# Kernel tuning notes

Hardware: AMD Instinct MI355X
Metric: run time of the kernel (lower is better)

The kernel has to match this reference:

```python
import jax, jax.numpy as jnp
import numpy as np

B, N_LR, N_HR, D, NH, L, K = 16, 256, 512, 512, 8, 4, 4
FF = 4 * D

def _ln(x, g, b):
    m = jnp.mean(x, -1, keepdims=True)
    v = jnp.var(x, -1, keepdims=True)
    return (x - m) * jax.lax.rsqrt(v + 1e-5) * g + b

def _gelu(x):
    return jax.nn.gelu(x, approximate=False)  # torch nn.GELU default = exact

def _attn(x, qkvW, qkvb, projW, projb, bias):
    b, n, d = x.shape
    hd = d // NH
    qkv = (x @ qkvW + qkvb).reshape(b, n, 3, NH, hd).transpose(2, 0, 3, 1, 4)
    q, k, v = qkv[0], qkv[1], qkv[2]
    a = jnp.einsum('bhnd,bhmd->bhnm', q, k) * (hd ** -0.5)
    if bias is not None:
        a = a + bias
    a = jax.nn.softmax(a, axis=-1)
    o = jnp.einsum('bhnm,bhmd->bhnd', a, v).transpose(0, 2, 1, 3).reshape(b, n, d)
    return o @ projW + projb

def _ffn(x, W1, b1, W2, b2):
    return _gelu(x @ W1 + b1) @ W2 + b2

def setup_inputs() -> dict:
    key = jax.random.key(0)
    ks = iter(jax.random.split(key, 64))
    def rn(shape, s=0.02):
        return jax.random.normal(next(ks), shape, jnp.float32) * s
    inp = {}
    A = rn((B, N_LR, N_LR), 1.0)
    A = 0.5 * (A + A.transpose(0, 2, 1))  # symmetric weighted adjacency
    inp['A_lr'] = A
    inp['X_lr'] = A  # node features = adjacency rows, as in the original model
    inp['ip_W'] = rn((N_LR, D)); inp['ip_b'] = jnp.zeros(D)
    inp['ip_g'] = jnp.ones(D); inp['ip_bt'] = jnp.zeros(D)
    inp['e_n1g'] = jnp.ones((L, D)); inp['e_n1b'] = jnp.zeros((L, D))
    inp['e_qkvW'] = rn((L, D, 3 * D)); inp['e_qkvb'] = jnp.zeros((L, 3 * D))
    inp['e_projW'] = rn((L, D, D)); inp['e_projb'] = jnp.zeros((L, D))
    inp['e_ebW'] = rn((L, NH), 1.0); inp['e_ebs'] = jnp.full((L,), 0.1)
    inp['e_n2g'] = jnp.ones((L, D)); inp['e_n2b'] = jnp.zeros((L, D))
    inp['e_f1W'] = rn((L, D, FF)); inp['e_f1b'] = jnp.zeros((L, FF))
    inp['e_f2W'] = rn((L, FF, D)); inp['e_f2b'] = jnp.zeros((L, D))
    inp['encn_g'] = jnp.ones(D); inp['encn_b'] = jnp.zeros(D)
    inp['up1W'] = rn((N_LR, N_HR)); inp['up1b'] = jnp.zeros(N_HR)
    inp['up2W'] = rn((N_HR, N_HR)); inp['up2b'] = jnp.zeros(N_HR)
    inp['r_n1g'] = jnp.ones(D); inp['r_n1b'] = jnp.zeros(D)
    inp['r_qkvW'] = rn((D, 3 * D)); inp['r_qkvb'] = jnp.zeros(3 * D)
    inp['r_projW'] = rn((D, D)); inp['r_projb'] = jnp.zeros(D)
    inp['r_n2g'] = jnp.ones(D); inp['r_n2b'] = jnp.zeros(D)
    inp['r_f1W'] = rn((D, FF)); inp['r_f1b'] = jnp.zeros(FF)
    inp['r_f2W'] = rn((FF, D)); inp['r_f2b'] = jnp.zeros(D)
    inp['hrn_g'] = jnp.ones(D); inp['hrn_b'] = jnp.zeros(D)
    inp['dec_W'] = rn((K, D, D)); inp['dec_b'] = jnp.full((1,), 3.0)
    return inp

def reference(A_lr, X_lr, ip_W, ip_b, ip_g, ip_bt, e_n1g, e_n1b, e_qkvW, e_qkvb, e_projW, e_projb, e_ebW, e_ebs, e_n2g, e_n2b, e_f1W, e_f1b, e_f2W, e_f2b, encn_g, encn_b, up1W, up1b, up2W, up2b, r_n1g, r_n1b, r_qkvW, r_qkvb, r_projW, r_projb, r_n2g, r_n2b, r_f1W, r_f1b, r_f2W, r_f2b, hrn_g, hrn_b, dec_W, dec_b):
    # input_proj: Linear -> LayerNorm -> GELU (dropout is identity in eval)
    H = _gelu(_ln(X_lr @ ip_W + ip_b, ip_g, ip_bt))  # (B, n_lr, D)
    # encoder: pre-norm blocks with additive per-head edge bias in softmax
    for l in range(L):
        bias = e_ebs[l] * A_lr[:, None, :, :] * e_ebW[l][None, :, None, None]  # (B,NH,N,N)
        H = H + _attn(_ln(H, e_n1g[l], e_n1b[l]), e_qkvW[l], e_qkvb[l], e_projW[l], e_projb[l], bias)
        H = H + _ffn(_ln(H, e_n2g[l], e_n2b[l]), e_f1W[l], e_f1b[l], e_f2W[l], e_f2b[l])
    H = _ln(H, encn_g, encn_b)
    # upsample n_lr -> n_hr along node axis (applied on transposed H)
    Ht = H.transpose(0, 2, 1)                      # (B, D, n_lr)
    Ht = _gelu(Ht @ up1W + up1b) @ up2W + up2b     # (B, D, n_hr)
    H = Ht.transpose(0, 2, 1)                      # (B, n_hr, D)
    # HR refinement: standard pre-norm self-attention block
    H = H + _attn(_ln(H, r_n1g, r_n1b), r_qkvW, r_qkvb, r_projW, r_projb, None)
    H = H + _ffn(_ln(H, r_n2g, r_n2b), r_f1W, r_f1b, r_f2W, r_f2b)
    H = _ln(H, hrn_g, hrn_b)
    # bilinear multi-head decoder: mean_k H W_k H^T, symmetrized
    A_pred = jnp.einsum('bnd,kde,bme->bnm', H, dec_W, H) / K
    A_pred = 0.5 * (A_pred + A_pred.transpose(0, 2, 1))
    iu, ju = np.triu_indices(N_HR, k=1)
    pred = A_pred[:, iu, ju]                        # (B, n_hr*(n_hr-1)/2)
    return jax.nn.softplus(pred + dec_b[0])
```

## Files before the change

### kernel.cpp

```cpp
#include <hip/hip_runtime.h>
#include <hip/hip_bf16.h>
#include <math.h>

#define DEV __device__ __forceinline__

typedef __attribute__((ext_vector_type(8))) short bf16x8;
typedef __attribute__((ext_vector_type(4))) short s16x4;
typedef __attribute__((ext_vector_type(4))) float f32x4;

DEV float gelu_f(float x) {
  float u = 1.5957691f * x * (1.0f + 0.044715f * x * x);
  return x / (1.0f + __expf(-u));
}

DEV short bf16s(float x) {
  __hip_bfloat16 v = __float2bfloat16(x);
  return *reinterpret_cast<short*>(&v);
}

DEV void async16(void* lds, const void* g) {
  __builtin_amdgcn_global_load_lds(
      (const __attribute__((address_space(1))) unsigned int*)g,
      (__attribute__((address_space(3))) unsigned int*)lds, 16, 0, 0);
}

__global__ __launch_bounds__(256) void conv2_kernel(
    const float* __restrict__ X1, __hip_bfloat16* __restrict__ Y1,
    const float* __restrict__ X2, __hip_bfloat16* __restrict__ Y2, int n) {
  int i = blockIdx.x * 256 + threadIdx.x;
  if (i < n) {
    Y1[i] = __float2bfloat16(X1[i]);
    Y2[i] = __float2bfloat16(X2[i]);
  }
}

struct CvArgs {
  const float* s[11];
  __hip_bfloat16* d[11];
};

__global__ __launch_bounds__(256) void multi_tconv_kernel(CvArgs a) {
  const int Rj[11] = {256, 512, 512, 512, 2048, 256, 512, 512, 512, 512, 2048};
  const int Cj[11] = {512, 1536, 512, 2048, 512, 512, 512, 1536, 512, 2048, 512};
  const int Nj[11] = {1, 4, 4, 4, 4, 1, 1, 1, 1, 1, 1};
  __shared__ float t[32][33];
  int rem = blockIdx.x, j = 0;
  for (; j < 11; ++j) {
    int tj = (Rj[j] >> 5) * (Cj[j] >> 5) * Nj[j];
    if (rem < tj) break;
    rem -= tj;
  }
  const int R = Rj[j], C = Cj[j];
  const int perb = (R >> 5) * (C >> 5);
  const int z = rem / perb;
  const int tt = rem % perb;
  const int tc = C >> 5;
  const int r0 = (tt / tc) << 5, c0 = (tt % tc) << 5;
  const float* xb = a.s[j] + (size_t)z * R * C;
  __hip_bfloat16* yb = a.d[j] + (size_t)z * R * C;
  int tx = threadIdx.x & 31, ty = threadIdx.x >> 5;
  for (int i = ty; i < 32; i += 8) t[i][tx] = xb[(size_t)(r0 + i) * C + c0 + tx];
  __syncthreads();
  for (int i = ty; i < 32; i += 8)
    yb[(size_t)(c0 + i) * R + r0 + tx] = __float2bfloat16(t[tx][i]);
}

__global__ __launch_bounds__(256) void build_s_kernel(
    const float* __restrict__ W, __hip_bfloat16* __restrict__ S, int D, int Kk) {
  int i = blockIdx.x * 256 + threadIdx.x;
  if (i >= D * D) return;
  int d = i / D, e = i % D;
  float s = 0.f;
  for (int k = 0; k < Kk; ++k) {
    s += W[(size_t)k * D * D + i];
    s += W[(size_t)k * D * D + (size_t)e * D + d];
  }
  S[i] = __float2bfloat16(s / (2.0f * Kk));
}

__global__ __launch_bounds__(256) void mgemm64_kernel(
    const __hip_bfloat16* __restrict__ A, const __hip_bfloat16* __restrict__ Bt,
    const float* __restrict__ bias, const float* __restrict__ resid,
    float* __restrict__ outf, __hip_bfloat16* __restrict__ outb,
    int M, int N, int K, int act, int mgrp) {
  __shared__ __align__(16) short As[2][64 * 64];
  __shared__ __align__(16) short Bs[2][64 * 64];
  const int tid = threadIdx.x;
  const int lane = tid & 63, wave = tid >> 6;
  const int quad = lane >> 4, l15 = lane & 15;
  const int bid = blockIdx.x;
  const int g = bid & 7, sidx = bid >> 3;
  const int mt = g * mgrp + sidx % mgrp;
  const int nt = sidx / mgrp;
  const int row0 = mt * 64, col0 = nt * 64;
  const short* Ag = (const short*)A;
  const short* Bg = (const short*)Bt;

  auto stage = [&](int bsel, int k0) {
#pragma unroll
    for (int i = 0; i < 2; ++i) {
      int c = (wave * 2 + i) * 64 + lane;
      int r = c >> 3, pp = c & 7;
      int kc = pp ^ (r & 7);
      async16(&As[bsel][(wave * 2 + i) * 512], &Ag[(size_t)(row0 + r) * K + k0 + kc * 8]);
      async16(&Bs[bsel][(wave * 2 + i) * 512], &Bg[(size_t)(col0 + r) * K + k0 + kc * 8]);
    }
  };

  f32x4 acc[4] = {};
  const int nk = K >> 6;
  stage(0, 0);
  for (int t = 0; t < nk; ++t) {
    const int cur = t & 1;
    __syncthreads();
    if (t + 1 < nk) stage(cur ^ 1, (t + 1) << 6);
#pragma unroll
    for (int kh = 0; kh < 2; ++kh) {
      const int ch = ((quad + kh * 4) ^ (l15 & 7)) * 8;
      bf16x8 af = *(const bf16x8*)&As[cur][(wave * 16 + l15) * 64 + ch];
#pragma unroll
      for (int ni = 0; ni < 4; ++ni) {
        bf16x8 bq = *(const bf16x8*)&Bs[cur][(ni * 16 + l15) * 64 + ch];
        acc[ni] = __builtin_amdgcn_mfma_f32_16x16x32_bf16(af, bq, acc[ni], 0, 0, 0);
      }
    }
  }

#pragma unroll
  for (int ni = 0; ni < 4; ++ni) {
    int cc = col0 + ni * 16 + l15;
    float bb = bias ? bias[cc] : 0.f;
#pragma unroll
    for (int r = 0; r < 4; ++r) {
      int rr = row0 + wave * 16 + quad * 4 + r;
      size_t idx = (size_t)rr * N + cc;
      float v = acc[ni][r] + bb;
      if (act) v = gelu_f(v);
      if (resid) v += resid[idx];
      if (outf) outf[idx] = v;
      if (outb) outb[idx] = __float2bfloat16(v);
    }
  }
}

__global__ __launch_bounds__(256) void mgemm128_kernel(
    const __hip_bfloat16* __restrict__ A, const __hip_bfloat16* __restrict__ Bt,
    const float* __restrict__ bias, const float* __restrict__ resid,
    float* __restrict__ outf, __hip_bfloat16* __restrict__ outb,
    int M, int N, int K, int act, int mgrp) {
  __shared__ __align__(16) short As[2][128 * 64];
  __shared__ __align__(16) short Bs[2][64 * 64];
  const int tid = threadIdx.x;
  const int lane = tid & 63, wave = tid >> 6;
  const int quad = lane >> 4, l15 = lane & 15;
  const int wr = wave >> 1, wc = wave & 1;
  const int bid = blockIdx.x;
  const int g = bid & 7, sidx = bid >> 3;
  const int mt = g * mgrp + sidx % mgrp;
  const int nt = sidx / mgrp;
  const int row0 = mt * 128, col0 = nt * 64;
  const short* Ag = (const short*)A;
  const short* Bg = (const short*)Bt;

  auto stage = [&](int bsel, int k0) {
#pragma unroll
    for (int i = 0; i < 4; ++i) {
      int c = i * 256 + tid;
      int r = c >> 3, pp = c & 7;
      int kc = pp ^ (r & 7);
      async16(&As[bsel][c * 8], &Ag[(size_t)(row0 + r) * K + k0 + kc * 8]);
    }
#pragma unroll
    for (int i = 0; i < 2; ++i) {
      int c = i * 256 + tid;
      int r = c >> 3, pp = c & 7;
      int kc = pp ^ (r & 7);
      async16(&Bs[bsel][c * 8], &Bg[(size_t)(col0 + r) * K + k0 + kc * 8]);
    }
  };

  f32x4 acc[4][2] = {};
  const int nk = K >> 6;
  stage(0, 0);
  for (int t = 0; t < nk; ++t) {
    const int cur = t & 1;
    __syncthreads();
    if (t + 1 < nk) stage(cur ^ 1, (t + 1) << 6);
#pragma unroll
    for (int kh = 0; kh < 2; ++kh) {
      const int ch = ((quad + kh * 4) ^ (l15 & 7)) * 8;
      bf16x8 af[4], bq[2];
#pragma unroll
      for (int mi = 0; mi < 4; ++mi)
        af[mi] = *(const bf16x8*)&As[cur][(wr * 64 + mi * 16 + l15) * 64 + ch];
#pragma unroll
      for (int ni = 0; ni < 2; ++ni)
        bq[ni] = *(const bf16x8*)&Bs[cur][(wc * 32 + ni * 16 + l15) * 64 + ch];
#pragma unroll
      for (int mi = 0; mi < 4; ++mi)
#pragma unroll
        for (int ni = 0; ni < 2; ++ni)
          acc[mi][ni] = __builtin_amdgcn_mfma_f32_16x16x32_bf16(af[mi], bq[ni], acc[mi][ni], 0, 0, 0);
    }
  }

#pragma unroll
  for (int ni = 0; ni < 2; ++ni) {
    int cc = col0 + wc * 32 + ni * 16 + l15;
    float bb = bias ? bias[cc] : 0.f;
#pragma unroll
    for (int mi = 0; mi < 4; ++mi) {
#pragma unroll
      for (int r = 0; r < 4; ++r) {
        int rr = row0 + wr * 64 + mi * 16 + quad * 4 + r;
        size_t idx = (size_t)rr * N + cc;
        float v = acc[mi][ni][r] + bb;
        if (act) v = gelu_f(v);
        if (resid) v += resid[idx];
        if (outf) outf[idx] = v;
        if (outb) outb[idx] = __float2bfloat16(v);
      }
    }
  }
}

__global__ __launch_bounds__(512) void mgemm_w8_kernel(
    const __hip_bfloat16* __restrict__ A, const __hip_bfloat16* __restrict__ Bt,
    const float* __restrict__ bias, const float* __restrict__ resid,
    float* __restrict__ outf, __hip_bfloat16* __restrict__ outb,
    int M, int N, int K, int act, int mgrp) {
  __shared__ __align__(16) short As[2][128 * 64];
  __shared__ __align__(16) short Bs[2][128 * 64];
  const int tid = threadIdx.x;
  const int lane = tid & 63, wave = tid >> 6;
  const int quad = lane >> 4, l15 = lane & 15;
  const int wr = wave >> 2, wc = wave & 3;
  const int bid = blockIdx.x;
  const int g = bid & 7, sidx = bid >> 3;
  const int mt = g * mgrp + sidx % mgrp;
  const int nt = sidx / mgrp;
  const int row0 = mt * 128, col0 = nt * 128;
  const short* Ag = (const short*)A;
  const short* Bg = (const short*)Bt;

  auto stage = [&](int bsel, int k0) {
#pragma unroll
    for (int i = 0; i < 2; ++i) {
      int c = i * 512 + tid;
      int r = c >> 3, pp = c & 7;
      int kc = pp ^ (r & 7);
      async16(&As[bsel][c * 8], &Ag[(size_t)(row0 + r) * K + k0 + kc * 8]);
    }
#pragma unroll
    for (int i = 0; i < 2; ++i) {
      int c = i * 512 + tid;
      int r = c >> 3, pp = c & 7;
      int kc = pp ^ (r & 7);
      async16(&Bs[bsel][c * 8], &Bg[(size_t)(col0 + r) * K + k0 + kc * 8]);
    }
  };

  f32x4 acc[4][2] = {};
  const int nk = K >> 6;
  stage(0, 0);
  for (int t = 0; t < nk; ++t) {
    const int cur = t & 1;
    __syncthreads();
    if (t + 1 < nk) stage(cur ^ 1, (t + 1) << 6);
#pragma unroll
    for (int kh = 0; kh < 2; ++kh) {
      const int ch = ((quad + kh * 4) ^ (l15 & 7)) * 8;
      bf16x8 af[4], bq[2];
#pragma unroll
      for (int mi = 0; mi < 4; ++mi)
        af[mi] = *(const bf16x8*)&As[cur][(wr * 64 + mi * 16 + l15) * 64 + ch];
#pragma unroll
      for (int ni = 0; ni < 2; ++ni)
        bq[ni] = *(const bf16x8*)&Bs[cur][(wc * 32 + ni * 16 + l15) * 64 + ch];
#pragma unroll
      for (int mi = 0; mi < 4; ++mi)
#pragma unroll
        for (int ni = 0; ni < 2; ++ni)
          acc[mi][ni] = __builtin_amdgcn_mfma_f32_16x16x32_bf16(af[mi], bq[ni], acc[mi][ni], 0, 0, 0);
    }
  }

#pragma unroll
  for (int ni = 0; ni < 2; ++ni) {
    int cc = col0 + wc * 32 + ni * 16 + l15;
    float bb = bias ? bias[cc] : 0.f;
#pragma unroll
    for (int mi = 0; mi < 4; ++mi) {
#pragma unroll
      for (int r = 0; r < 4; ++r) {
        int rr = row0 + wr * 64 + mi * 16 + quad * 4 + r;
        size_t idx = (size_t)rr * N + cc;
        float v = acc[mi][ni][r] + bb;
        if (act) v = gelu_f(v);
        if (resid) v += resid[idx];
        if (outf) outf[idx] = v;
        if (outb) outb[idx] = __float2bfloat16(v);
      }
    }
  }
}

__global__ __launch_bounds__(256) void qkv_gemm_kernel(
    const __hip_bfloat16* __restrict__ A, const __hip_bfloat16* __restrict__ Bt,
    const float* __restrict__ bias, __hip_bfloat16* __restrict__ qkv,
    int M, int K, int nseq, int lgn, int mgrp) {
  __shared__ __align__(16) short As[2][128 * 64];
  __shared__ __align__(16) short Bs[2][64 * 64];
  const int tid = threadIdx.x;
  const int lane = tid & 63, wave = tid >> 6;
  const int quad = lane >> 4, l15 = lane & 15;
  const int wr = wave >> 1, wc = wave & 1;
  const int bid = blockIdx.x;
  const int g = bid & 7, sidx = bid >> 3;
  const int mt = g * mgrp + sidx % mgrp;
  const int nt = sidx / mgrp;
  const int row0 = mt * 128, col0 = nt * 64;
  const short* Ag = (const short*)A;
  const short* Bg = (const short*)Bt;

  auto stage = [&](int bsel, int k0) {
#pragma unroll
    for (int i = 0; i < 4; ++i) {
      int c = i * 256 + tid;
      int r = c >> 3, pp = c & 7;
      int kc = pp ^ (r & 7);
      async16(&As[bsel][c * 8], &Ag[(size_t)(row0 + r) * K + k0 + kc * 8]);
    }
#pragma unroll
    for (int i = 0; i < 2; ++i) {
      int c = i * 256 + tid;
      int r = c >> 3, pp = c & 7;
      int kc = pp ^ (r & 7);
      async16(&Bs[bsel][c * 8], &Bg[(size_t)(col0 + r) * K + k0 + kc * 8]);
    }
  };

  f32x4 acc[4][2] = {};
  const int nk = K >> 6;
  stage(0, 0);
  for (int t = 0; t < nk; ++t) {
    const int cur = t & 1;
    __syncthreads();
    if (t + 1 < nk) stage(cur ^ 1, (t + 1) << 6);
#pragma unroll
    for (int kh = 0; kh < 2; ++kh) {
      const int ch = ((quad + kh * 4) ^ (l15 & 7)) * 8;
      bf16x8 af[4], bq[2];
#pragma unroll
      for (int mi = 0; mi < 4; ++mi)
        af[mi] = *(const bf16x8*)&As[cur][(wr * 64 + mi * 16 + l15) * 64 + ch];
#pragma unroll
      for (int ni = 0; ni < 2; ++ni)
        bq[ni] = *(const bf16x8*)&Bs[cur][(wc * 32 + ni * 16 + l15) * 64 + ch];
#pragma unroll
      for (int mi = 0; mi < 4; ++mi)
#pragma unroll
        for (int ni = 0; ni < 2; ++ni)
          acc[mi][ni] = __builtin_amdgcn_mfma_f32_16x16x32_bf16(af[mi], bq[ni], acc[mi][ni], 0, 0, 0);
    }
  }

  const size_t PART = (size_t)M * 512;
#pragma unroll
  for (int ni = 0; ni < 2; ++ni) {
    int cc = col0 + wc * 32 + ni * 16 + l15;
    float bb = bias ? bias[cc] : 0.f;
    int which = cc >> 9;
    int h = (cc >> 6) & 7;
    int d = cc & 63;
#pragma unroll
    for (int mi = 0; mi < 4; ++mi) {
#pragma unroll
      for (int r = 0; r < 4; ++r) {
        int rr = row0 + wr * 64 + mi * 16 + quad * 4 + r;
        int b = rr >> lgn;
        int nn = rr & (nseq - 1);
        float v = acc[mi][ni][r] + bb;
        size_t dst;
        if (which == 2) {
          dst = 2 * PART + (((size_t)b * 8 + h) * 64 + d) * nseq + nn;
        } else {
          dst = (size_t)which * PART + (((size_t)b * 8 + h) * nseq + nn) * 64 + d;
        }
        qkv[dst] = __float2bfloat16(v);
      }
    }
  }
}

__global__ __launch_bounds__(256) void fattn_kernel(
    const __hip_bfloat16* __restrict__ Qh, const __hip_bfloat16* __restrict__ Kh,
    const __hip_bfloat16* __restrict__ Vt, __hip_bfloat16* __restrict__ O,
    const __hip_bfloat16* __restrict__ Abias, const float* __restrict__ ebW,
    const float* __restrict__ ebs, int N, int lgq) {
  __shared__ __align__(16) short Ks[2][64 * 64];
  __shared__ __align__(16) short Vs[2][64 * 64];
  __shared__ __align__(16) short Ps[4][16][72];
  const int bid = blockIdx.x;
  const int g = bid & 7, s = bid >> 3;
  const int bloc = s >> (lgq + 3);
  const int rem = s & ((8 << lgq) - 1);
  const int h = rem >> lgq;
  const int qt = rem & ((1 << lgq) - 1);
  const int b = g * 2 + bloc;
  const int tid = threadIdx.x, lane = tid & 63, wave = tid >> 6;
  const int quad = lane >> 4, l15 = lane & 15;
  const size_t hb = (size_t)b * 8 + h;
  const short* Qg = (const short*)Qh + hb * N * 64;
  const short* Kg = (const short*)Kh + hb * N * 64;
  const short* Vg = (const short*)Vt + hb * 64 * N;
  const float scale = 0.125f;
  const bool hasb = (Abias != nullptr);
  const float bscale = hasb ? ebs[0] * ebW[h] : 0.f;
  const int qrow_w = qt * 64 + wave * 16;

  auto stageKV = [&](int bsel, int k0) {
#pragma unroll
    for (int i = 0; i < 2; ++i) {
      int c = (wave * 2 + i) * 64 + lane;
      int r = c >> 3, pp = c & 7;
      int kc = pp ^ (r & 7);
      async16(&Ks[bsel][(wave * 2 + i) * 512], &Kg[(size_t)(k0 + r) * 64 + kc * 8]);
      async16(&Vs[bsel][(wave * 2 + i) * 512], &Vg[(size_t)r * N + k0 + kc * 8]);
    }
  };

  bf16x8 qf[2];
  qf[0] = *(const bf16x8*)&Qg[(size_t)(qrow_w + l15) * 64 + quad * 8];
  qf[1] = *(const bf16x8*)&Qg[(size_t)(qrow_w + l15) * 64 + quad * 8 + 32];

  float l_r[4] = {0.f, 0.f, 0.f, 0.f};
  f32x4 oacc[4] = {};

  const int ntl = N >> 6;
  stageKV(0, 0);
  for (int t = 0; t < ntl; ++t) {
    const int cur = t & 1;
    const int k0 = t << 6;
    __syncthreads();
    if (t + 1 < ntl) stageKV(cur ^ 1, (t + 1) << 6);

    f32x4 sv[4] = {};
    __builtin_amdgcn_s_setprio(1);
#pragma unroll
    for (int kh = 0; kh < 2; ++kh) {
      const int ch = ((quad + kh * 4) ^ (l15 & 7)) * 8;
#pragma unroll
      for (int ni = 0; ni < 4; ++ni) {
        bf16x8 kf = *(const bf16x8*)&Ks[cur][(ni * 16 + l15) * 64 + ch];
        sv[ni] = __builtin_amdgcn_mfma_f32_16x16x32_bf16(qf[kh], kf, sv[ni], 0, 0, 0);
      }
    }
    __builtin_amdgcn_s_setprio(0);
    if (hasb) {
#pragma unroll
      for (int ni = 0; ni < 4; ++ni)
#pragma unroll
        for (int r = 0; r < 4; ++r) {
          int qq = qrow_w + quad * 4 + r;
          int kk = k0 + ni * 16 + l15;
          float ab = __bfloat162float(Abias[((size_t)b * N + qq) * N + kk]);
          sv[ni][r] = sv[ni][r] * scale + bscale * ab;
        }
    } else {
#pragma unroll
      for (int ni = 0; ni < 4; ++ni)
#pragma unroll
        for (int r = 0; r < 4; ++r) sv[ni][r] *= scale;
    }

#pragma unroll
    for (int ni = 0; ni < 4; ++ni)
#pragma unroll
      for (int r = 0; r < 4; ++r) {
        float p = __expf(sv[ni][r]);
        sv[ni][r] = p;
        l_r[r] += p;
      }

#pragma unroll
    for (int ni = 0; ni < 4; ++ni)
#pragma unroll
      for (int r = 0; r < 4; ++r)
        Ps[wave][quad * 4 + r][ni * 16 + l15] = bf16s(sv[ni][r]);

    bf16x8 pf0 = *(const bf16x8*)&Ps[wave][l15][quad * 8];
    bf16x8 pf1 = *(const bf16x8*)&Ps[wave][l15][quad * 8 + 32];
    __builtin_amdgcn_s_setprio(1);
#pragma unroll
    for (int kh = 0; kh < 2; ++kh) {
      const int ch = ((quad + kh * 4) ^ (l15 & 7)) * 8;
#pragma unroll
      for (int ni = 0; ni < 4; ++ni) {
        bf16x8 vf = *(const bf16x8*)&Vs[cur][(ni * 16 + l15) * 64 + ch];
        oacc[ni] = __builtin_amdgcn_mfma_f32_16x16x32_bf16(kh ? pf1 : pf0, vf, oacc[ni], 0, 0, 0);
      }
    }
    __builtin_amdgcn_s_setprio(0);
  }

#pragma unroll
  for (int off = 1; off < 16; off <<= 1)
#pragma unroll
    for (int r = 0; r < 4; ++r) l_r[r] += __shfl_xor(l_r[r], off, 64);
  float inv[4];
#pragma unroll
  for (int r = 0; r < 4; ++r) inv[r] = 1.f / l_r[r];
#pragma unroll
  for (int ni = 0; ni < 4; ++ni)
#pragma unroll
    for (int r = 0; r < 4; ++r) {
      int nn = qrow_w + quad * 4 + r;
      int col = h * 64 + ni * 16 + l15;
      O[((size_t)b * N + nn) * 512 + col] = __float2bfloat16(oacc[ni][r] * inv[r]);
    }
}

__global__ __launch_bounds__(256) void dec_mfma_kernel(
    const __hip_bfloat16* __restrict__ Tb_, const __hip_bfloat16* __restrict__ Hb_,
    const float* __restrict__ dec_b, float* __restrict__ out) {
  const int Nn = 512, K = 512;
  __shared__ __align__(16) short As[2][64 * 64];
  __shared__ __align__(16) short Bs[2][64 * 64];
  int p = blockIdx.x;
  int bb = blockIdx.y;
  int it = 0, rem = p;
  while (rem >= 8 - it) { rem -= 8 - it; ++it; }
  int jt = it + rem;
  const int row0 = it * 64, col0 = jt * 64;
  const int tid = threadIdx.x;
  const int lane = tid & 63, wave = tid >> 6;
  const int quad = lane >> 4, l15 = lane & 15;
  const int wr = (wave >> 1) * 32, wc = (wave & 1) * 32;
  const short* Ag = (const short*)(Tb_ + (size_t)bb * Nn * K);
  const short* Bg = (const short*)(Hb_ + (size_t)bb * Nn * K);

  auto stage = [&](int bsel, int k0) {
#pragma unroll
    for (int i = 0; i < 2; ++i) {
      int c = (wave * 2 + i) * 64 + lane;
      int r = c >> 3, pp = c & 7;
      int kc = pp ^ (r & 7);
      async16(&As[bsel][(wave * 2 + i) * 512], &Ag[(size_t)(row0 + r) * K + k0 + kc * 8]);
      async16(&Bs[bsel][(wave * 2 + i) * 512], &Bg[(size_t)(col0 + r) * K + k0 + kc * 8]);
    }
  };

  f32x4 acc[2][2] = {};
  const int nk = K >> 6;
  stage(0, 0);
  for (int t = 0; t < nk; ++t) {
    const int cur = t & 1;
    __syncthreads();
    if (t + 1 < nk) stage(cur ^ 1, (t + 1) << 6);
#pragma unroll
    for (int kh = 0; kh < 2; ++kh) {
      const int ch = ((quad + kh * 4) ^ (l15 & 7)) * 8;
      bf16x8 af[2], bq[2];
#pragma unroll
      for (int mi = 0; mi < 2; ++mi)
        af[mi] = *(const bf16x8*)&As[cur][(wr + mi * 16 + l15) * 64 + ch];
#pragma unroll
      for (int ni = 0; ni < 2; ++ni)
        bq[ni] = *(const bf16x8*)&Bs[cur][(wc + ni * 16 + l15) * 64 + ch];
#pragma unroll
      for (int mi = 0; mi < 2; ++mi)
#pragma unroll
        for (int ni = 0; ni < 2; ++ni)
          acc[mi][ni] = __builtin_amdgcn_mfma_f32_16x16x32_bf16(af[mi], bq[ni], acc[mi][ni], 0, 0, 0);
    }
  }

  float db = dec_b[0];
  size_t obase = (size_t)bb * ((size_t)Nn * (Nn - 1) / 2);
#pragma unroll
  for (int mi = 0; mi < 2; ++mi) {
#pragma unroll
    for (int ni = 0; ni < 2; ++ni) {
      int j = col0 + wc + ni * 16 + l15;
#pragma unroll
      for (int r = 0; r < 4; ++r) {
        int i = row0 + wr + mi * 16 + quad * 4 + r;
        if (j > i) {
          float x = acc[mi][ni][r] + db;
          float sp = fmaxf(x, 0.f) + __logf(1.f + __expf(-fabsf(x)));
          out[obase + (size_t)i * (2 * Nn - i - 1) / 2 + (j - i - 1)] = sp;
        }
      }
    }
  }
}

__global__ __launch_bounds__(256) void ln_kernel(
    const float* __restrict__ X, float* __restrict__ outf,
    __hip_bfloat16* __restrict__ outb, const float* __restrict__ g,
    const float* __restrict__ b, int do_gelu) {
  const int row = blockIdx.x * 4 + (threadIdx.x >> 6);
  const int lane = threadIdx.x & 63;
  const float4* x = (const float4*)X + (size_t)row * 128;
  float4 v0 = x[lane], v1 = x[lane + 64];
  float s = v0.x + v0.y + v0.z + v0.w + v1.x + v1.y + v1.z + v1.w;
  float s2 = v0.x * v0.x + v0.y * v0.y + v0.z * v0.z + v0.w * v0.w +
             v1.x * v1.x + v1.y * v1.y + v1.z * v1.z + v1.w * v1.w;
#pragma unroll
  for (int off = 32; off; off >>= 1) {
    s += __shfl_xor(s, off, 64);
    s2 += __shfl_xor(s2, off, 64);
  }
  const float mean = s * (1.0f / 512.0f);
  const float inv = rsqrtf(s2 * (1.0f / 512.0f) - mean * mean + 1e-5f);
  const float4 g0 = ((const float4*)g)[lane], g1 = ((const float4*)g)[lane + 64];
  const float4 b0 = ((const float4*)b)[lane], b1 = ((const float4*)b)[lane + 64];
  float4 y0, y1;
  y0.x = (v0.x - mean) * inv * g0.x + b0.x;
  y0.y = (v0.y - mean) * inv * g0.y + b0.y;
  y0.z = (v0.z - mean) * inv * g0.z + b0.z;
  y0.w = (v0.w - mean) * inv * g0.w + b0.w;
  y1.x = (v1.x - mean) * inv * g1.x + b1.x;
  y1.y = (v1.y - mean) * inv * g1.y + b1.y;
  y1.z = (v1.z - mean) * inv * g1.z + b1.z;
  y1.w = (v1.w - mean) * inv * g1.w + b1.w;
  if (do_gelu) {
    y0.x = gelu_f(y0.x); y0.y = gelu_f(y0.y); y0.z = gelu_f(y0.z); y0.w = gelu_f(y0.w);
    y1.x = gelu_f(y1.x); y1.y = gelu_f(y1.y); y1.z = gelu_f(y1.z); y1.w = gelu_f(y1.w);
  }
  if (outf) {
    float4* of = (float4*)outf + (size_t)row * 128;
    of[lane] = y0;
    of[lane + 64] = y1;
  }
  if (outb) {
    s16x4 p0, p1;
    p0.x = bf16s(y0.x); p0.y = bf16s(y0.y); p0.z = bf16s(y0.z); p0.w = bf16s(y0.w);
    p1.x = bf16s(y1.x); p1.y = bf16s(y1.y); p1.z = bf16s(y1.z); p1.w = bf16s(y1.w);
    *(s16x4*)((short*)outb + (size_t)row * 512 + lane * 4) = p0;
    *(s16x4*)((short*)outb + (size_t)row * 512 + 256 + lane * 4) = p1;
  }
}

template <typename T>
__global__ __launch_bounds__(256) void transpose_kernel(
    const T* __restrict__ X, T* __restrict__ Y, int R, int C) {
  __shared__ T t[32][33];
  const T* xb = X + (size_t)blockIdx.z * R * C;
  T* yb = Y + (size_t)blockIdx.z * R * C;
  int c0 = blockIdx.x * 32, r0 = blockIdx.y * 32;
  int tx = threadIdx.x & 31, ty = threadIdx.x >> 5;
  for (int i = ty; i < 32; i += 8) t[i][tx] = xb[(size_t)(r0 + i) * C + c0 + tx];
  __syncthreads();
  for (int i = ty; i < 32; i += 8) yb[(size_t)(c0 + i) * R + r0 + tx] = t[tx][i];
}

extern "C" void kernel_launch(void* const* d_in, const int* in_sizes, int n_in,
                              void* d_out, int out_size, void* d_ws, size_t ws_size,
                              hipStream_t stream) {
  const float *A_lr = (const float*)d_in[0], *X_lr = (const float*)d_in[1],
              *ip_W = (const float*)d_in[2], *ip_b = (const float*)d_in[3],
              *ip_g = (const float*)d_in[4], *ip_bt = (const float*)d_in[5],
              *e_n1g = (const float*)d_in[6], *e_n1b = (const float*)d_in[7],
              *e_qkvW = (const float*)d_in[8], *e_qkvb = (const float*)d_in[9],
              *e_projW = (const float*)d_in[10], *e_projb = (const float*)d_in[11],
              *e_ebW = (const float*)d_in[12], *e_ebs = (const float*)d_in[13],
              *e_n2g = (const float*)d_in[14], *e_n2b = (const float*)d_in[15],
              *e_f1W = (const float*)d_in[16], *e_f1b = (const float*)d_in[17],
              *e_f2W = (const float*)d_in[18], *e_f2b = (const float*)d_in[19],
              *encn_g = (const float*)d_in[20], *encn_b = (const float*)d_in[21],
              *up1W = (const float*)d_in[22], *up1b = (const float*)d_in[23],
              *up2W = (const float*)d_in[24], *up2b = (const float*)d_in[25],
              *r_n1g = (const float*)d_in[26], *r_n1b = (const float*)d_in[27],
              *r_qkvW = (const float*)d_in[28], *r_qkvb = (const float*)d_in[29],
              *r_projW = (const float*)d_in[30], *r_projb = (const float*)d_in[31],
              *r_n2g = (const float*)d_in[32], *r_n2b = (const float*)d_in[33],
              *r_f1W = (const float*)d_in[34], *r_f1b = (const float*)d_in[35],
              *r_f2W = (const float*)d_in[36], *r_f2b = (const float*)d_in[37],
              *hrn_g = (const float*)d_in[38], *hrn_b = (const float*)d_in[39],
              *dec_W = (const float*)d_in[40], *dec_b = (const float*)d_in[41];

  const int Bb = 16, NLR = 256, NHR = 512, Dm = 512, NHh = 8, FF = 2048, Ll = 4;
  typedef __hip_bfloat16 bf;

  float* ws = (float*)d_ws;
  float* H = ws;
  float* Hf = ws + 4194304;
  bf* XNb = (bf*)(ws + 8388608);
  bf* AOb = (bf*)(ws + 10485760);
  bf* BIGb = (bf*)(ws + 12582912);
  bf* WB = (bf*)(ws + 20971520);
  bf* Xlrb = (bf*)(ws + 29229056);
  bf* Albrb = (bf*)(ws + 29753344);

  size_t o = 0;
  bf* ipWt = WB + o;   o += (size_t)512 * 256;
  bf* eqkvT = WB + o;  o += (size_t)4 * 1536 * 512;
  bf* eprojT = WB + o; o += (size_t)4 * 512 * 512;
  bf* ef1T = WB + o;   o += (size_t)4 * 2048 * 512;
  bf* ef2T = WB + o;   o += (size_t)4 * 512 * 2048;
  bf* up1T = WB + o;   o += (size_t)512 * 256;
  bf* up2T = WB + o;   o += (size_t)512 * 512;
  bf* rqkvT = WB + o;  o += (size_t)1536 * 512;
  bf* rprojT = WB + o; o += (size_t)512 * 512;
  bf* rf1T = WB + o;   o += (size_t)2048 * 512;
  bf* rf2T = WB + o;   o += (size_t)512 * 2048;
  bf* Sb = WB + o;     o += (size_t)512 * 512;

  bf* Q_e = BIGb;
  bf* K_e = BIGb + 2097152;
  bf* V_e = BIGb + 4194304;
  bf* Q_r = BIGb;
  bf* K_r = BIGb + 4194304;
  bf* V_r = BIGb + 8388608;

  CvArgs cv;
  cv.s[0] = ip_W;   cv.d[0] = ipWt;
  cv.s[1] = e_qkvW; cv.d[1] = eqkvT;
  cv.s[2] = e_projW; cv.d[2] = eprojT;
  cv.s[3] = e_f1W;  cv.d[3] = ef1T;
  cv.s[4] = e_f2W;  cv.d[4] = ef2T;
  cv.s[5] = up1W;   cv.d[5] = up1T;
  cv.s[6] = up2W;   cv.d[6] = up2T;
  cv.s[7] = r_qkvW; cv.d[7] = rqkvT;
  cv.s[8] = r_projW; cv.d[8] = rprojT;
  cv.s[9] = r_f1W;  cv.d[9] = rf1T;
  cv.s[10] = r_f2W; cv.d[10] = rf2T;
  multi_tconv_kernel<<<15872, 256, 0, stream>>>(cv);
  conv2_kernel<<<(1048576 + 255) / 256, 256, 0, stream>>>(
      X_lr, Xlrb, A_lr, Albrb, 1048576);
  build_s_kernel<<<(512 * 512 + 255) / 256, 256, 0, stream>>>(dec_W, Sb, Dm, 4);

  mgemm64_kernel<<<512, 256, 0, stream>>>(
      Xlrb, ipWt, ip_b, nullptr, Hf, nullptr, Bb * NLR, Dm, NLR, 0, 8);
  ln_kernel<<<Bb * NLR / 4, 256, 0, stream>>>(Hf, H, nullptr, ip_g, ip_bt, 1);

  for (int l = 0; l < Ll; ++l) {
    ln_kernel<<<Bb * NLR / 4, 256, 0, stream>>>(H, nullptr, XNb, e_n1g + l * Dm, e_n1b + l * Dm, 0);
    qkv_gemm_kernel<<<768, 256, 0, stream>>>(
        XNb, eqkvT + (size_t)l * 1536 * 512, e_qkvb + l * 1536, BIGb,
        Bb * NLR, Dm, NLR, 8, 4);
    fattn_kernel<<<16 * 8 * 4, 256, 0, stream>>>(
        Q_e, K_e, V_e, AOb, Albrb, e_ebW + l * NHh, e_ebs + l, NLR, 2);
    mgemm64_kernel<<<512, 256, 0, stream>>>(
        AOb, eprojT + (size_t)l * 512 * 512, e_projb + l * Dm, H,
        H, nullptr, Bb * NLR, Dm, Dm, 0, 8);
    ln_kernel<<<Bb * NLR / 4, 256, 0, stream>>>(H, nullptr, XNb, e_n2g + l * Dm, e_n2b + l * Dm, 0);
    mgemm_w8_kernel<<<512, 512, 0, stream>>>(
        XNb, ef1T + (size_t)l * 2048 * 512, e_f1b + l * FF, nullptr,
        nullptr, BIGb, Bb * NLR, FF, Dm, 1, 4);
    mgemm64_kernel<<<512, 256, 0, stream>>>(
        BIGb, ef2T + (size_t)l * 512 * 2048, e_f2b + l * Dm, H,
        H, nullptr, Bb * NLR, Dm, FF, 0, 8);
  }

  ln_kernel<<<Bb * NLR / 4, 256, 0, stream>>>(H, nullptr, XNb, encn_g, encn_b, 0);
  transpose_kernel<bf><<<dim3(16, 8, Bb), 256, 0, stream>>>(XNb, AOb, NLR, Dm);
  mgemm128_kernel<<<512, 256, 0, stream>>>(
      AOb, up1T, up1b, nullptr, nullptr, BIGb, Bb * Dm, NHR, NLR, 1, 8);
  mgemm128_kernel<<<512, 256, 0, stream>>>(
      BIGb, up2T, up2b, nullptr, Hf, nullptr, Bb * Dm, NHR, NHR, 0, 8);
  transpose_kernel<float><<<dim3(16, 16, Bb), 256, 0, stream>>>(Hf, H, Dm, NHR);

  ln_kernel<<<Bb * NHR / 4, 256, 0, stream>>>(H, nullptr, XNb, r_n1g, r_n1b, 0);
  qkv_gemm_kernel<<<1536, 256, 0, stream>>>(
      XNb, rqkvT, r_qkvb, BIGb, Bb * NHR, Dm, NHR, 9, 8);
  fattn_kernel<<<16 * 8 * 8, 256, 0, stream>>>(
      Q_r, K_r, V_r, AOb, nullptr, nullptr, nullptr, NHR, 3);
  mgemm128_kernel<<<512, 256, 0, stream>>>(
      AOb, rprojT, r_projb, H, H, nullptr, Bb * NHR, Dm, Dm, 0, 8);
  ln_kernel<<<Bb * NHR / 4, 256, 0, stream>>>(H, nullptr, XNb, r_n2g, r_n2b, 0);
  mgemm_w8_kernel<<<1024, 512, 0, stream>>>(
      XNb, rf1T, r_f1b, nullptr, nullptr, BIGb, Bb * NHR, FF, Dm, 1, 8);
  mgemm128_kernel<<<512, 256, 0, stream>>>(
      BIGb, rf2T, r_f2b, H, H, nullptr, Bb * NHR, Dm, FF, 0, 8);

  ln_kernel<<<Bb * NHR / 4, 256, 0, stream>>>(H, nullptr, XNb, hrn_g, hrn_b, 0);
  mgemm128_kernel<<<512, 256, 0, stream>>>(
      XNb, Sb, nullptr, nullptr, nullptr, AOb, Bb * NHR, Dm, Dm, 0, 8);
  dec_mfma_kernel<<<dim3(36, Bb), 256, 0, stream>>>(
      AOb, XNb, dec_b, (float*)d_out);
}
```

Measured before the change: 797.7 us.

## Add triple-buffered 64x64 GEMM with vmcnt waits and use for N=512 GEMMs

Adds a new 64x64-tile GEMM kernel that keeps three LDS buffers and two async load stages in flight. It waits on the hardware vmcnt counter instead of a full __syncthreads, so loads overlap more of the MFMA work. The encoder proj/ffn2 GEMMs switch to it, and several HR-stage GEMMs move from 128-wide tiles to 64-wide tiles with twice as many blocks. Smaller tiles give more parallelism but less data reuse, and the extra buffer raises LDS usage.

```diff
diff --git a/kernel.cpp b/kernel.cpp
--- a/kernel.cpp
+++ b/kernel.cpp
@@ -124,6 +124,78 @@
         acc[ni] = __builtin_amdgcn_mfma_f32_16x16x32_bf16(af, bq, acc[ni], 0, 0, 0);
       }
     }
+  }
+
+#pragma unroll
+  for (int ni = 0; ni < 4; ++ni) {
+    int cc = col0 + ni * 16 + l15;
+    float bb = bias ? bias[cc] : 0.f;
+#pragma unroll
+    for (int r = 0; r < 4; ++r) {
+      int rr = row0 + wave * 16 + quad * 4 + r;
+      size_t idx = (size_t)rr * N + cc;
+      float v = acc[ni][r] + bb;
+      if (act) v = gelu_f(v);
+      if (resid) v += resid[idx];
+      if (outf) outf[idx] = v;
+      if (outb) outb[idx] = __float2bfloat16(v);
+    }
+  }
+}
+
+__global__ __launch_bounds__(256) void mgemm64p_kernel(
+    const __hip_bfloat16* __restrict__ A, const __hip_bfloat16* __restrict__ Bt,
+    const float* __restrict__ bias, const float* __restrict__ resid,
+    float* __restrict__ outf, __hip_bfloat16* __restrict__ outb,
+    int M, int N, int K, int act, int mgrp) {
+  __shared__ __align__(16) short As[3][64 * 64];
+  __shared__ __align__(16) short Bs[3][64 * 64];
+  const int tid = threadIdx.x;
+  const int lane = tid & 63, wave = tid >> 6;
+  const int quad = lane >> 4, l15 = lane & 15;
+  const int bid = blockIdx.x;
+  const int g = bid & 7, sidx = bid >> 3;
+  const int mt = g * mgrp + sidx % mgrp;
+  const int nt = sidx / mgrp;
+  const int row0 = mt * 64, col0 = nt * 64;
+  const short* Ag = (const short*)A;
+  const short* Bg = (const short*)Bt;
+
+  auto stage = [&](int bsel, int k0) {
+#pragma unroll
+    for (int i = 0; i < 2; ++i) {
+      int c = (wave * 2 + i) * 64 + lane;
+      int r = c >> 3, pp = c & 7;
+      int kc = pp ^ (r & 7);
+      async16(&As[bsel][(wave * 2 + i) * 512], &Ag[(size_t)(row0 + r) * K + k0 + kc * 8]);
+      async16(&Bs[bsel][(wave * 2 + i) * 512], &Bg[(size_t)(col0 + r) * K + k0 + kc * 8]);
+    }
+  };
+
+  f32x4 acc[4] = {};
+  const int nk = K >> 6;
+  stage(0, 0);
+  stage(1, 64);
+  int cur = 0, nb = 2;
+  for (int t = 0; t < nk; ++t) {
+    if (t + 1 < nk)
+      asm volatile("s_waitcnt vmcnt(4)" ::: "memory");
+    else
+      asm volatile("s_waitcnt vmcnt(0)" ::: "memory");
+    __builtin_amdgcn_s_barrier();
+    if (t + 2 < nk) stage(nb, (t + 2) << 6);
+#pragma unroll
+    for (int kh = 0; kh < 2; ++kh) {
+      const int ch = ((quad + kh * 4) ^ (l15 & 7)) * 8;
+      bf16x8 af = *(const bf16x8*)&As[cur][(wave * 16 + l15) * 64 + ch];
+#pragma unroll
+      for (int ni = 0; ni < 4; ++ni) {
+        bf16x8 bq = *(const bf16x8*)&Bs[cur][(ni * 16 + l15) * 64 + ch];
+        acc[ni] = __builtin_amdgcn_mfma_f32_16x16x32_bf16(af, bq, acc[ni], 0, 0, 0);
+      }
+    }
+    cur = (cur == 2) ? 0 : cur + 1;
+    nb = (nb == 2) ? 0 : nb + 1;
   }
 
 #pragma unroll
@@ -743,14 +815,14 @@
         Bb * NLR, Dm, NLR, 8, 4);
     fattn_kernel<<<16 * 8 * 4, 256, 0, stream>>>(
         Q_e, K_e, V_e, AOb, Albrb, e_ebW + l * NHh, e_ebs + l, NLR, 2);
-    mgemm64_kernel<<<512, 256, 0, stream>>>(
+    mgemm64p_kernel<<<512, 256, 0, stream>>>(
         AOb, eprojT + (size_t)l * 512 * 512, e_projb + l * Dm, H,
         H, nullptr, Bb * NLR, Dm, Dm, 0, 8);
     ln_kernel<<<Bb * NLR / 4, 256, 0, stream>>>(H, nullptr, XNb, e_n2g + l * Dm, e_n2b + l * Dm, 0);
     mgemm_w8_kernel<<<512, 512, 0, stream>>>(
         XNb, ef1T + (size_t)l * 2048 * 512, e_f1b + l * FF, nullptr,
         nullptr, BIGb, Bb * NLR, FF, Dm, 1, 4);
-    mgemm64_kernel<<<512, 256, 0, stream>>>(
+    mgemm64p_kernel<<<512, 256, 0, stream>>>(
         BIGb, ef2T + (size_t)l * 512 * 2048, e_f2b + l * Dm, H,
         H, nullptr, Bb * NLR, Dm, FF, 0, 8);
   }
@@ -759,8 +831,8 @@
   transpose_kernel<bf><<<dim3(16, 8, Bb), 256, 0, stream>>>(XNb, AOb, NLR, Dm);
   mgemm128_kernel<<<512, 256, 0, stream>>>(
       AOb, up1T, up1b, nullptr, nullptr, BIGb, Bb * Dm, NHR, NLR, 1, 8);
-  mgemm128_kernel<<<512, 256, 0, stream>>>(
-      BIGb, up2T, up2b, nullptr, Hf, nullptr, Bb * Dm, NHR, NHR, 0, 8);
+  mgemm64p_kernel<<<1024, 256, 0, stream>>>(
+      BIGb, up2T, up2b, nullptr, Hf, nullptr, Bb * Dm, NHR, NHR, 0, 16);
   transpose_kernel<float><<<dim3(16, 16, Bb), 256, 0, stream>>>(Hf, H, Dm, NHR);
 
   ln_kernel<<<Bb * NHR / 4, 256, 0, stream>>>(H, nullptr, XNb, r_n1g, r_n1b, 0);
@@ -768,17 +840,17 @@
       XNb, rqkvT, r_qkvb, BIGb, Bb * NHR, Dm, NHR, 9, 8);
   fattn_kernel<<<16 * 8 * 8, 256, 0, stream>>>(
       Q_r, K_r, V_r, AOb, nullptr, nullptr, nullptr, NHR, 3);
-  mgemm128_kernel<<<512, 256, 0, stream>>>(
-      AOb, rprojT, r_projb, H, H, nullptr, Bb * NHR, Dm, Dm, 0, 8);
+  mgemm64p_kernel<<<1024, 256, 0, stream>>>(
+      AOb, rprojT, r_projb, H, H, nullptr, Bb * NHR, Dm, Dm, 0, 16);
   ln_kernel<<<Bb * NHR / 4, 256, 0, stream>>>(H, nullptr, XNb, r_n2g, r_n2b, 0);
   mgemm_w8_kernel<<<1024, 512, 0, stream>>>(
       XNb, rf1T, r_f1b, nullptr, nullptr, BIGb, Bb * NHR, FF, Dm, 1, 8);
-  mgemm128_kernel<<<512, 256, 0, stream>>>(
-      BIGb, rf2T, r_f2b, H, H, nullptr, Bb * NHR, Dm, FF, 0, 8);
+  mgemm64p_kernel<<<1024, 256, 0, stream>>>(
+      BIGb, rf2T, r_f2b, H, H, nullptr, Bb * NHR, Dm, FF, 0, 16);
 
   ln_kernel<<<Bb * NHR / 4, 256, 0, stream>>>(H, nullptr, XNb, hrn_g, hrn_b, 0);
-  mgemm128_kernel<<<512, 256, 0, stream>>>(
-      XNb, Sb, nullptr, nullptr, nullptr, AOb, Bb * NHR, Dm, Dm, 0, 8);
+  mgemm64p_kernel<<<1024, 256, 0, stream>>>(
+      XNb, Sb, nullptr, nullptr, nullptr, AOb, Bb * NHR, Dm, Dm, 0, 16);
   dec_mfma_kernel<<<dim3(36, Bb), 256, 0, stream>>>(
       AOb, XNb, dec_b, (float*)d_out);
 }
```

Result: slower. 830.5 us (+4.1%).
